# Kernel tuning notes

Hardware: AMD Instinct MI355X
Metric: run time of the kernel (lower is better)

## Reference

```python
import jax, jax.numpy as jnp
import numpy as np

MODE = 'max'  # matches init kwarg `mode`
EPS = 1e-6

def before_after(x):
    n, d = x.shape
    zero = jnp.zeros((1, d), dtype=x.dtype)
    if MODE == 'max':
        # exclusive prefix max (x_before[0] = 0, matching torch.zeros_like base)
        pre = jax.lax.cummax(x, axis=0)
        before = jnp.concatenate([zero, pre[:-1]], axis=0)
        suf = jax.lax.cummax(x[::-1], axis=0)[::-1]
        after = jnp.concatenate([suf[1:], zero], axis=0)
    else:  # mean
        cs = jnp.cumsum(x, axis=0)
        cnt_b = jnp.arange(1, n, dtype=x.dtype)[:, None]
        before = jnp.concatenate([zero, cs[:-1] / cnt_b], axis=0)
        total = cs[-1]
        cnt_a = jnp.arange(n - 1, 0, -1, dtype=x.dtype)[:, None]
        after = jnp.concatenate([(total[None, :] - cs[:-1]) / cnt_a, zero], axis=0)
    return before, after

def setup_inputs() -> dict:
    key = jax.random.key(0)
    ks = jax.random.split(key, 6)
    n, dim, dff = 8192, 1024, 4096
    s1 = 1.0 / np.sqrt(3 * dim)
    s2 = 1.0 / np.sqrt(dff)
    return {
        'x': jax.random.normal(ks[0], (n, dim), jnp.float32),
        'W1': jax.random.normal(ks[1], (dff, 3 * dim), jnp.float32) * s1,
        'b1': jax.random.normal(ks[2], (dff,), jnp.float32) * s1,
        'ln_w': jnp.ones((dff,), jnp.float32),
        'ln_b': jnp.zeros((dff,), jnp.float32),
        'W2': jax.random.normal(ks[3], (dim, dff), jnp.float32) * s2,
        'b2': jax.random.normal(ks[4], (dim,), jnp.float32) * s2,
        'gamma': jnp.full((dim,), 1e-6, jnp.float32),
    }

def reference(x, W1, b1, ln_w, ln_b, W2, b2, gamma):
    shortcut = x
    before, after = before_after(x)
    h = jnp.concatenate([x, before, after], axis=1)          # [n, 3*dim]
    h = jax.nn.relu(h @ W1.T + b1)                           # [n, dff]
    mu = jnp.mean(h, axis=-1, keepdims=True)
    var = jnp.mean(jnp.square(h - mu), axis=-1, keepdims=True)
    h = (h - mu) * jax.lax.rsqrt(var + EPS) * ln_w + ln_b
    # dropout is identity in eval mode
    out = h @ W2.T + b2                                      # [n, dim]
    return out * gamma[None, :] + shortcut
```

## Files before the change

kernel.cpp:

```cpp
#include <hip/hip_runtime.h>

typedef __attribute__((ext_vector_type(4))) float f32x4;
typedef __attribute__((ext_vector_type(8))) short s16x8;
typedef __attribute__((ext_vector_type(8))) unsigned short u16x8;

#define AS1(p) ((const __attribute__((address_space(1))) void*)(p))
#define AS3(p) ((__attribute__((address_space(3))) void*)(p))

__device__ __forceinline__ unsigned short f2bf(float f) {
  unsigned u = __builtin_bit_cast(unsigned, f);
  u += 0x7fffu + ((u >> 16) & 1u);
  return (unsigned short)(u >> 16);
}
__device__ __forceinline__ float bf2f(unsigned short s) {
  unsigned u = ((unsigned)s) << 16;
  return __builtin_bit_cast(float, u);
}
__device__ __forceinline__ unsigned f2e4m3(float f) {
  unsigned uf = __builtin_bit_cast(unsigned, f);
  unsigned s = (uf >> 24) & 0x80u;
  unsigned u = uf & 0x7fffffffu;
  if (u < 0x3c800000u) return s;
  if (u > 0x43e00000u) u = 0x43e00000u;
  u += 0x7ffffu + ((u >> 20) & 1u);
  unsigned v = (u >> 20) - 960u;
  if (v > 126u) v = 126u;
  return s | v;
}


__global__ __launch_bounds__(256) void cast_weights(const float* __restrict__ W1,
                                                    unsigned char* __restrict__ W1q,
                                                    long n1,
                                                    const float* __restrict__ W2,
                                                    unsigned char* __restrict__ W2q,
                                                    long n2) {
  if (blockIdx.x < 1536) {
    long i = ((long)blockIdx.x * 256 + threadIdx.x) * 4;
    long stride = (long)1536 * 256 * 4;
    for (; i < n1; i += stride) {
      float4 f = *(const float4*)(W1 + i);
      unsigned v = f2e4m3(f.x * 32.f) | (f2e4m3(f.y * 32.f) << 8) |
                   (f2e4m3(f.z * 32.f) << 16) | (f2e4m3(f.w * 32.f) << 24);
      long n = i / 3072;
      long k = i - n * 3072;
      long phys = n * 3072 + (k & ~(long)127) + ((k & 127) ^ ((n & 15) << 3));
      *(unsigned*)(W1q + phys) = v;
    }
  } else {
    long i = ((long)(blockIdx.x - 1536) * 256 + threadIdx.x) * 4;
    long stride = (long)512 * 256 * 4;
    for (; i < n2; i += stride) {
      float4 f = *(const float4*)(W2 + i);
      unsigned v = f2e4m3(f.x * 32.f) | (f2e4m3(f.y * 32.f) << 8) |
                   (f2e4m3(f.z * 32.f) << 16) | (f2e4m3(f.w * 32.f) << 24);
      long n = i >> 12;
      long k = i & 4095;
      long phys = (n << 12) + (k & ~(long)127) + ((k & 127) ^ ((n & 15) << 3));
      *(unsigned*)(W2q + phys) = v;
    }
  }
}

__global__ __launch_bounds__(256) void w2_fold(const float* __restrict__ W2,
                                               const float* __restrict__ lnw,
                                               const float* __restrict__ lnb,
                                               float* __restrict__ w2l,
                                               float* __restrict__ b2l) {
  const int n = blockIdx.x;
  const float* w = W2 + (long)n * 4096;
  float s = 0.f, b = 0.f;
  for (int k = threadIdx.x; k < 4096; k += 256) {
    float wv = w[k];
    s += wv * lnw[k];
    b += wv * lnb[k];
  }
#pragma unroll
  for (int off = 32; off; off >>= 1) {
    s += __shfl_xor(s, off, 64);
    b += __shfl_xor(b, off, 64);
  }
  __shared__ float ss[4], bb[4];
  const int wv2 = threadIdx.x >> 6;
  if ((threadIdx.x & 63) == 0) { ss[wv2] = s; bb[wv2] = b; }
  __syncthreads();
  if (threadIdx.x == 0) {
    w2l[n] = ss[0] + ss[1] + ss[2] + ss[3];
    b2l[n] = bb[0] + bb[1] + bb[2] + bb[3];
  }
}

__global__ __launch_bounds__(256) void scan_chunkmax(const float* __restrict__ x,
                                                     float* __restrict__ partial) {
  int col = blockIdx.x * 256 + threadIdx.x;
  int chunk = blockIdx.y;
  const float* p = x + (long)chunk * 64 * 1024 + col;
  float m = -INFINITY;
#pragma unroll 4
  for (int i = 0; i < 64; i++) m = fmaxf(m, p[(long)i * 1024]);
  partial[chunk * 1024 + col] = m;
}

__global__ __launch_bounds__(256) void scan_chunkscan(const float* __restrict__ partial,
                                                      float* __restrict__ prefix,
                                                      float* __restrict__ suffix) {
  int col = blockIdx.x * 256 + threadIdx.x;
  float v[128];
#pragma unroll
  for (int c = 0; c < 128; c++) v[c] = partial[c * 1024 + col];
  float run = -INFINITY;
#pragma unroll
  for (int c = 0; c < 128; c++) {
    prefix[c * 1024 + col] = run;
    run = fmaxf(run, v[c]);
  }
  run = -INFINITY;
#pragma unroll
  for (int c = 127; c >= 0; c--) {
    suffix[c * 1024 + col] = run;
    run = fmaxf(run, v[c]);
  }
}

__global__ __launch_bounds__(256) void scan_emit(const float* __restrict__ x,
                                                 const float* __restrict__ prefix,
                                                 const float* __restrict__ suffix,
                                                 unsigned char* __restrict__ h_in) {
  int col = blockIdx.x * 256 + threadIdx.x;
  int chunk = blockIdx.y;
  long r0 = (long)chunk * 64;
  const int cb = col & ~127, cw = col & 127;
  float run = prefix[chunk * 1024 + col];
  for (int i = 0; i < 64; i++) {
    long row = r0 + i;
    int xo = (int)(row & 15) << 3;
    int c0 = cb | (cw ^ xo);
    float v = x[row * 1024 + col];
    unsigned char* hr = h_in + row * 3072;
    hr[c0] = (unsigned char)f2e4m3(v);
    hr[1024 + c0] = (unsigned char)(row == 0 ? 0u : f2e4m3(run));
    run = fmaxf(run, v);
  }
  float run2 = suffix[chunk * 1024 + col];
  for (int i = 63; i >= 0; i--) {
    long row = r0 + i;
    int xo = (int)(row & 15) << 3;
    int c0 = cb | (cw ^ xo);
    float v = x[row * 1024 + col];
    h_in[row * 3072 + 2048 + c0] = (unsigned char)(row == 8191 ? 0u : f2e4m3(run2));
    run2 = fmaxf(run2, v);
  }
}

__global__ __launch_bounds__(256) void ln_stats_reduce(const float* __restrict__ pp,
                                                       float* __restrict__ rowstats) {
  int row = blockIdx.x * 256 + threadIdx.x;
  int tm = row >> 8, rl = row & 255;
  float s = 0.f, q = 0.f;
#pragma unroll
  for (int tn = 0; tn < 16; ++tn) {
    const float* p = pp + (((long)(tm * 16 + tn) * 256 + rl) * 2);
    s += p[0];
    q += p[1];
  }
  float mu = s * (1.f / 4096.f);
  float var = q * (1.f / 4096.f) - mu * mu;
  rowstats[row * 2] = mu;
  rowstats[row * 2 + 1] = rsqrtf(var + 1e-6f);
}

__global__ __launch_bounds__(512, 2) void gemm256_relu(
    const unsigned char* __restrict__ A, const unsigned char* __restrict__ B,
    unsigned char* __restrict__ C, const float* __restrict__ bias,
    const float* __restrict__ lnw, float* __restrict__ pp,
    int M, int N, int K) {
  extern __shared__ char smem[];
  const int NT = K >> 7;

  const int nwg = gridDim.x;
  const int cpx = nwg >> 3;
  const int bid = blockIdx.x;
  const int swz = (bid & 7) * cpx + (bid >> 3);
  const int tiles_m = M >> 8;
  const int tm = swz % tiles_m;
  const int tn = swz / tiles_m;
  const long brow = (long)tm * 256;
  const long bcol = (long)tn * 256;

  const int t = threadIdx.x;
  const int lane = t & 63, wv = t >> 6;
  const int wr = wv >> 2, wc = wv & 3;
  const int fr = lane & 15, fk = lane >> 4;

  const int srow = t >> 3;
  const int scol = (t & 7) * 16;
  const unsigned char* Asrc = A + (brow + srow) * (long)K + scol;
  const unsigned char* Bsrc = B + (bcol + srow) * (long)K + scol;
  const long hstep = (long)128 * K, lstep = (long)64 * K;

#define STAGE_A(j, reg, h, L)                                                   \
  __builtin_amdgcn_global_load_lds(AS1(Asrc + (h)*hstep + (L)*lstep + (j)*128), \
      AS3(smem + (reg)*32768 + (h)*16384 + (L)*8192 + t * 16), 16, 0, 0)
#define STAGE_B(j, h, L)                                                        \
  __builtin_amdgcn_global_load_lds(AS1(Bsrc + (h)*hstep + (L)*lstep + (j)*128), \
      AS3(smem + 98304 + ((j)&1) * 32768 + (h)*16384 + (L)*8192 + t * 16), 16, 0, 0)

  const int xr = fr << 3;
  const char* ArdRow = smem + (wr * 128 + fr) * 128;
  const char* BrdRow = smem + 98304 + (wc * 64 + fr) * 128;
#define RD_A(ar_, m, kk) \
  (*(const long*)(ArdRow + (ar_)*32768 + (m)*2048 + (((kk)*32 + fk * 8) ^ xr)))
#define RD_B(pb_, n, kk) \
  (*(const long*)(BrdRow + (pb_)*32768 + (n)*2048 + (((kk)*32 + fk * 8) ^ xr)))

#define MFMA_QUAD(mi, a_)                                                      \
  _Pragma("unroll")                                                            \
  for (int n = 0; n < 4; ++n) {                                                \
    _Pragma("unroll")                                                          \
    for (int kk = 0; kk < 4; ++kk)                                             \
      acc[(mi)][n] = __builtin_amdgcn_mfma_f32_16x16x32_fp8_fp8(               \
          a_[kk], bfr[n][kk], acc[(mi)][n], 0, 0, 0);                          \
  }

  f32x4 acc[8][4];
#pragma unroll
  for (int m = 0; m < 8; m++)
#pragma unroll
    for (int n = 0; n < 4; n++) acc[m][n] = (f32x4)0.f;

  STAGE_A(0, 0, 0, 0); STAGE_A(0, 0, 0, 1); STAGE_A(0, 0, 1, 0); STAGE_A(0, 0, 1, 1);
  STAGE_B(0, 0, 0); STAGE_B(0, 0, 1); STAGE_B(0, 1, 0); STAGE_B(0, 1, 1);
  STAGE_A(1, 1, 0, 0); STAGE_A(1, 1, 0, 1); STAGE_A(1, 1, 1, 0); STAGE_A(1, 1, 1, 1);
  STAGE_B(1, 0, 0); STAGE_B(1, 0, 1); STAGE_B(1, 1, 0); STAGE_B(1, 1, 1);
  asm volatile("s_waitcnt vmcnt(8)" ::: "memory");
  __builtin_amdgcn_s_barrier();

  long bfr[4][4];
  long ap[2][2][4];
  ap[0][0][0] = RD_A(0, 0, 0); ap[0][0][1] = RD_A(0, 0, 1);
  ap[0][0][2] = RD_A(0, 0, 2); ap[0][0][3] = RD_A(0, 0, 3);
  ap[0][1][0] = RD_A(0, 1, 0); ap[0][1][1] = RD_A(0, 1, 1);
  ap[0][1][2] = RD_A(0, 1, 2); ap[0][1][3] = RD_A(0, 1, 3);

  int ar = 0;
  for (int g = 0; g < NT; ++g) {
    const int pb = g & 1;
    int sr = ar + 2; if (sr >= 3) sr -= 3;
    int nar = ar + 1; if (nar >= 3) nar = 0;
    const bool st = (g + 2 < NT);
#pragma unroll
    for (int p = 0; p < 4; ++p) {
      const int cs = p & 1, ns = cs ^ 1;
      if (p == 0) {
#pragma unroll
        for (int n = 0; n < 4; ++n)
#pragma unroll
          for (int kk = 0; kk < 4; ++kk) bfr[n][kk] = RD_B(pb, n, kk);
      }
      asm volatile("s_waitcnt lgkmcnt(0)" ::: "memory");
      __builtin_amdgcn_sched_barrier(0);
      __builtin_amdgcn_s_setprio(1);
      MFMA_QUAD(2 * p, ap[cs][0])
      MFMA_QUAD(2 * p + 1, ap[cs][1])
      __builtin_amdgcn_s_setprio(0);
      if (p < 3) {
#pragma unroll
        for (int kk = 0; kk < 4; ++kk) {
          ap[ns][0][kk] = RD_A(ar, 2 * p + 2, kk);
          ap[ns][1][kk] = RD_A(ar, 2 * p + 3, kk);
        }
      } else if (g + 1 < NT) {
#pragma unroll
        for (int kk = 0; kk < 4; ++kk) {
          ap[ns][0][kk] = RD_A(nar, 0, kk);
          ap[ns][1][kk] = RD_A(nar, 1, kk);
        }
      }
      if (st) {
        if (p == 0) { STAGE_A(g + 2, sr, 0, 0); STAGE_A(g + 2, sr, 0, 1); }
        if (p == 1) { STAGE_A(g + 2, sr, 1, 0); STAGE_A(g + 2, sr, 1, 1); }
        if (p == 2) { STAGE_B(g + 2, 0, 0); STAGE_B(g + 2, 0, 1); }
        if (p == 3) { STAGE_B(g + 2, 1, 0); STAGE_B(g + 2, 1, 1); }
      }
      if (p == 2 && g + 1 < NT) {
        if (st) asm volatile("s_waitcnt vmcnt(6)" ::: "memory");
        else    asm volatile("s_waitcnt vmcnt(0)" ::: "memory");
      }
      asm volatile("s_barrier" ::: "memory");
    }
    ar = nar;
  }

  float bi[4], lw[4];
#pragma unroll
  for (int n = 0; n < 4; ++n) {
    const long col = bcol + wc * 64 + n * 16 + fr;
    bi[n] = bias[col];
    lw[n] = lnw[col];
  }
  float* sred = (float*)smem;
  float* qred = sred + 1024;
  const long orow = brow + wr * 128 + fk * 4;
  const int ocol = (int)bcol + wc * 64 + fr;
#pragma unroll
  for (int m = 0; m < 8; ++m) {
#pragma unroll
    for (int r = 0; r < 4; ++r) {
      const long row = orow + m * 16 + r;
      const int xo = ((fk * 4 + r) & 15) << 3;
      float s = 0.f, q = 0.f;
#pragma unroll
      for (int n = 0; n < 4; ++n) {
        float v = acc[m][n][r] * 0.03125f + bi[n];
        v = v > 0.f ? v : 0.f;
        s += v;
        q += v * v;
        const int col = ocol + n * 16;
        const int phys = (col & ~127) | ((col & 127) ^ xo);
        C[row * (long)N + phys] = (unsigned char)f2e4m3(v * lw[n]);
      }
#pragma unroll
      for (int off = 1; off < 16; off <<= 1) {
        s += __shfl_xor(s, off, 64);
        q += __shfl_xor(q, off, 64);
      }
      if (fr == 0) {
        int rl = wr * 128 + m * 16 + fk * 4 + r;
        sred[rl * 4 + wc] = s;
        qred[rl * 4 + wc] = q;
      }
    }
  }
  __syncthreads();
  if (t < 256) {
    float s = sred[t * 4] + sred[t * 4 + 1] + sred[t * 4 + 2] + sred[t * 4 + 3];
    float q = qred[t * 4] + qred[t * 4 + 1] + qred[t * 4 + 2] + qred[t * 4 + 3];
    float* pb = pp + (((long)(tm * 16 + tn) * 256 + t) * 2);
    pb[0] = s;
    pb[1] = q;
  }
#undef STAGE_A
#undef STAGE_B
#undef RD_A
#undef RD_B
#undef MFMA_QUAD
}

__global__ __launch_bounds__(512, 2) void gemm256_g2(
    const unsigned char* __restrict__ A, const unsigned char* __restrict__ B,
    float* __restrict__ Cf, const float* __restrict__ bias,
    const float* __restrict__ gamma, const float* __restrict__ resid,
    const float* __restrict__ w2l, const float* __restrict__ b2l,
    const float* __restrict__ rowstats,
    int M, int N, int K) {
  extern __shared__ char smem[];
  const int NT = K >> 7;

  const int nwg = gridDim.x;
  const int cpx = nwg >> 3;
  const int bid = blockIdx.x;
  const int swz = (bid & 7) * cpx + (bid >> 3);
  const int tiles_m = M >> 8;
  const int tm = swz % tiles_m;
  const int tn = swz / tiles_m;
  const long brow = (long)tm * 256;
  const long bcol = (long)tn * 128;

  const int t = threadIdx.x;
  const int lane = t & 63, wv = t >> 6;
  const int wr = wv >> 1, wc = wv & 1;
  const int fr = lane & 15, fk = lane >> 4;

  const int srow = t >> 3;
  const int scol = (t & 7) * 16;
  const unsigned char* Asrc = A + (brow + srow) * (long)K + scol;
  const unsigned char* Bsrc = B + (bcol + srow) * (long)K + scol;
  const long hstep = (long)128 * K, lstep = (long)64 * K;

#define STAGE_A2(j, reg, h, L)                                                  \
  __builtin_amdgcn_global_load_lds(AS1(Asrc + (h)*hstep + (L)*lstep + (j)*128), \
      AS3(smem + (reg)*32768 + (h)*16384 + (L)*8192 + t * 16), 16, 0, 0)
#define STAGE_B2(j, L)                                                          \
  __builtin_amdgcn_global_load_lds(AS1(Bsrc + (L)*lstep + (j)*128),             \
      AS3(smem + 98304 + ((j)&1) * 16384 + (L)*8192 + t * 16), 16, 0, 0)

  const int xr = fr << 3;
  const char* ArdRow = smem + (wr * 64 + fr) * 128;
  const char* BrdRow = smem + 98304 + (wc * 64 + fr) * 128;
#define RD_A2(ar_, m, kk) \
  (*(const long*)(ArdRow + (ar_)*32768 + (m)*2048 + (((kk)*32 + fk * 8) ^ xr)))
#define RD_B2(pb_, n, kk) \
  (*(const long*)(BrdRow + (pb_)*16384 + (n)*2048 + (((kk)*32 + fk * 8) ^ xr)))

  f32x4 acc[4][4];
#pragma unroll
  for (int m = 0; m < 4; m++)
#pragma unroll
    for (int n = 0; n < 4; n++) acc[m][n] = (f32x4)0.f;

  STAGE_A2(0, 0, 0, 0); STAGE_A2(0, 0, 0, 1); STAGE_A2(0, 0, 1, 0); STAGE_A2(0, 0, 1, 1);
  STAGE_B2(0, 0); STAGE_B2(0, 1);
  STAGE_A2(1, 1, 0, 0); STAGE_A2(1, 1, 0, 1); STAGE_A2(1, 1, 1, 0); STAGE_A2(1, 1, 1, 1);
  STAGE_B2(1, 0); STAGE_B2(1, 1);
  asm volatile("s_waitcnt vmcnt(6)" ::: "memory");
  __builtin_amdgcn_s_barrier();

  long bfr[4][4];
  long ap[2][4];
  ap[0][0] = RD_A2(0, 0, 0); ap[0][1] = RD_A2(0, 0, 1);
  ap[0][2] = RD_A2(0, 0, 2); ap[0][3] = RD_A2(0, 0, 3);

  int ar = 0;
  for (int g = 0; g < NT; ++g) {
    const int pb = g & 1;
    int sr = ar + 2; if (sr >= 3) sr -= 3;
    int nar = ar + 1; if (nar >= 3) nar = 0;
    const bool st = (g + 2 < NT);
#pragma unroll
    for (int p = 0; p < 4; ++p) {
      const int cs = p & 1, ns = cs ^ 1;
      if (p == 0) {
#pragma unroll
        for (int n = 0; n < 4; ++n)
#pragma unroll
          for (int kk = 0; kk < 4; ++kk) bfr[n][kk] = RD_B2(pb, n, kk);
      }
      asm volatile("s_waitcnt lgkmcnt(0)" ::: "memory");
      __builtin_amdgcn_sched_barrier(0);
      __builtin_amdgcn_s_setprio(1);
#pragma unroll
      for (int n = 0; n < 4; ++n)
#pragma unroll
        for (int kk = 0; kk < 4; ++kk)
          acc[p][n] = __builtin_amdgcn_mfma_f32_16x16x32_fp8_fp8(
              ap[cs][kk], bfr[n][kk], acc[p][n], 0, 0, 0);
      __builtin_amdgcn_s_setprio(0);
      if (p < 3) {
#pragma unroll
        for (int kk = 0; kk < 4; ++kk) ap[ns][kk] = RD_A2(ar, p + 1, kk);
      } else if (g + 1 < NT) {
#pragma unroll
        for (int kk = 0; kk < 4; ++kk) ap[ns][kk] = RD_A2(nar, 0, kk);
      }
      if (st) {
        if (p == 0) { STAGE_A2(g + 2, sr, 0, 0); STAGE_A2(g + 2, sr, 0, 1); }
        if (p == 1) { STAGE_A2(g + 2, sr, 1, 0); STAGE_A2(g + 2, sr, 1, 1); }
        if (p == 2) { STAGE_B2(g + 2, 0); STAGE_B2(g + 2, 1); }
      }
      if (p == 2 && g + 1 < NT) {
        if (st) asm volatile("s_waitcnt vmcnt(6)" ::: "memory");
        else    asm volatile("s_waitcnt vmcnt(0)" ::: "memory");
      }
      asm volatile("s_barrier" ::: "memory");
    }
    ar = nar;
  }

  float bi[4], ga[4], wl[4], bl[4];
#pragma unroll
  for (int n = 0; n < 4; ++n) {
    const long col = bcol + wc * 64 + n * 16 + fr;
    bi[n] = bias[col];
    ga[n] = gamma[col];
    wl[n] = w2l[col];
    bl[n] = b2l[col];
  }
  const long orow = brow + wr * 64 + fk * 4;
  const long ocol = bcol + wc * 64 + fr;
#pragma unroll
  for (int m = 0; m < 4; ++m)
#pragma unroll
    for (int r = 0; r < 4; ++r) {
      const long row = orow + m * 16 + r;
      const float mu = rowstats[row * 2];
      const float rs = rowstats[row * 2 + 1];
#pragma unroll
      for (int n = 0; n < 4; ++n) {
        const long col = ocol + n * 16;
        float v = rs * (acc[m][n][r] * 0.03125f) - rs * mu * wl[n] + bl[n] + bi[n];
        Cf[row * (long)N + col] = v * ga[n] + resid[row * (long)N + col];
      }
    }
#undef STAGE_A2
#undef STAGE_B2
#undef RD_A2
#undef RD_B2
}

extern "C" void kernel_launch(void* const* d_in, const int* in_sizes, int n_in,
                              void* d_out, int out_size, void* d_ws, size_t ws_size,
                              hipStream_t stream) {
  const float* x     = (const float*)d_in[0];
  const float* W1    = (const float*)d_in[1];
  const float* b1    = (const float*)d_in[2];
  const float* ln_w  = (const float*)d_in[3];
  const float* ln_b  = (const float*)d_in[4];
  const float* W2    = (const float*)d_in[5];
  const float* b2    = (const float*)d_in[6];
  const float* gamma = (const float*)d_in[7];
  float* out = (float*)d_out;

  const int Nr = 8192, DIM = 1024, DFF = 4096, K1 = 3072;

  unsigned char* W1q   = (unsigned char*)d_ws;
  unsigned char* W2q   = W1q + (long)DFF * K1;
  unsigned char* h_in  = W2q + (long)DIM * DFF;
  unsigned char* h_act = h_in + (long)Nr * K1;
  float* partial  = (float*)(h_act + (long)Nr * DFF);
  float* prefix   = partial + 128 * 1024;
  float* suffix   = prefix + 128 * 1024;
  float* pp       = suffix + 128 * 1024;
  float* rowstats = pp + 32 * 16 * 256 * 2;
  float* w2l      = rowstats + (long)Nr * 2;
  float* b2l      = w2l + DIM;

  hipFuncSetAttribute((const void*)gemm256_relu,
                      hipFuncAttributeMaxDynamicSharedMemorySize, 163840);
  hipFuncSetAttribute((const void*)gemm256_g2,
                      hipFuncAttributeMaxDynamicSharedMemorySize, 131072);

  cast_weights<<<2048, 256, 0, stream>>>(W1, W1q, (long)DFF * K1,
                                         W2, W2q, (long)DIM * DFF);

  scan_chunkmax<<<dim3(4, 128), 256, 0, stream>>>(x, partial);
  scan_chunkscan<<<4, 256, 0, stream>>>(partial, prefix, suffix);
  scan_emit<<<dim3(4, 128), 256, 0, stream>>>(x, prefix, suffix, h_in);

  w2_fold<<<DIM, 256, 0, stream>>>(W2, ln_w, ln_b, w2l, b2l);

  gemm256_relu<<<512, 512, 163840, stream>>>(h_in, W1q, h_act, b1, ln_w, pp,
                                             Nr, DFF, K1);

  ln_stats_reduce<<<32, 256, 0, stream>>>(pp, rowstats);

  gemm256_g2<<<256, 512, 131072, stream>>>(h_act, W2q, out, b2, gamma, x,
                                           w2l, b2l, rowstats, Nr, DIM, DFF);
}
```

Baseline: 297.2 us.

## Merge prep kernels and fold scan and LN-stats reduction into consumers

Combines weight casting, chunk-max, and W2 LayerNorm folding into one prep launch. The chunk-level prefix/suffix scan is dropped: each scan_emit thread now reads all 128 chunk partials and computes its own exclusive prefix and suffix max. The separate LN-stats reduction kernel is removed, and the second GEMM reduces per-row partial sums into shared memory in its epilogue. This cuts the launch count from 8 to 4 and removes small serial kernels, at the cost of redundant partial reads in scan_emit and a block barrier in the GEMM epilogue.

```diff
diff --git a/kernel.cpp b/kernel.cpp
--- a/kernel.cpp
+++ b/kernel.cpp
@@ -1,8 +1,6 @@
 #include <hip/hip_runtime.h>
 
 typedef __attribute__((ext_vector_type(4))) float f32x4;
-typedef __attribute__((ext_vector_type(8))) short s16x8;
-typedef __attribute__((ext_vector_type(8))) unsigned short u16x8;
 
 #define AS1(p) ((const __attribute__((address_space(1))) void*)(p))
 #define AS3(p) ((__attribute__((address_space(3))) void*)(p))
@@ -11,10 +9,6 @@
   unsigned u = __builtin_bit_cast(unsigned, f);
   u += 0x7fffu + ((u >> 16) & 1u);
   return (unsigned short)(u >> 16);
-}
-__device__ __forceinline__ float bf2f(unsigned short s) {
-  unsigned u = ((unsigned)s) << 16;
-  return __builtin_bit_cast(float, u);
 }
 __device__ __forceinline__ unsigned f2e4m3(float f) {
   unsigned uf = __builtin_bit_cast(unsigned, f);
@@ -29,15 +23,22 @@
 }
 
 
-__global__ __launch_bounds__(256) void cast_weights(const float* __restrict__ W1,
-                                                    unsigned char* __restrict__ W1q,
-                                                    long n1,
-                                                    const float* __restrict__ W2,
-                                                    unsigned char* __restrict__ W2q,
-                                                    long n2) {
-  if (blockIdx.x < 1536) {
-    long i = ((long)blockIdx.x * 256 + threadIdx.x) * 4;
-    long stride = (long)1536 * 256 * 4;
+__global__ __launch_bounds__(256) void prep(const float* __restrict__ W1,
+                                            unsigned char* __restrict__ W1q,
+                                            const float* __restrict__ W2,
+                                            unsigned char* __restrict__ W2q,
+                                            const float* __restrict__ x,
+                                            float* __restrict__ partial,
+                                            const float* __restrict__ lnw,
+                                            const float* __restrict__ lnb,
+                                            float* __restrict__ w2l,
+                                            float* __restrict__ b2l) {
+  __shared__ float ss[4], bb[4];
+  const int bid = blockIdx.x;
+  if (bid < 1536) {
+    long i = ((long)bid * 256 + threadIdx.x) * 4;
+    const long n1 = (long)4096 * 3072;
+    const long stride = (long)1536 * 256 * 4;
     for (; i < n1; i += stride) {
       float4 f = *(const float4*)(W1 + i);
       unsigned v = f2e4m3(f.x * 32.f) | (f2e4m3(f.y * 32.f) << 8) |
@@ -47,9 +48,10 @@
       long phys = n * 3072 + (k & ~(long)127) + ((k & 127) ^ ((n & 15) << 3));
       *(unsigned*)(W1q + phys) = v;
     }
-  } else {
-    long i = ((long)(blockIdx.x - 1536) * 256 + threadIdx.x) * 4;
-    long stride = (long)512 * 256 * 4;
+  } else if (bid < 2048) {
+    long i = ((long)(bid - 1536) * 256 + threadIdx.x) * 4;
+    const long n2 = (long)1024 * 4096;
+    const long stride = (long)512 * 256 * 4;
     for (; i < n2; i += stride) {
       float4 f = *(const float4*)(W2 + i);
       unsigned v = f2e4m3(f.x * 32.f) | (f2e4m3(f.y * 32.f) << 8) |
@@ -59,78 +61,54 @@
       long phys = (n << 12) + (k & ~(long)127) + ((k & 127) ^ ((n & 15) << 3));
       *(unsigned*)(W2q + phys) = v;
     }
-  }
-}
-
-__global__ __launch_bounds__(256) void w2_fold(const float* __restrict__ W2,
-                                               const float* __restrict__ lnw,
-                                               const float* __restrict__ lnb,
-                                               float* __restrict__ w2l,
-                                               float* __restrict__ b2l) {
-  const int n = blockIdx.x;
-  const float* w = W2 + (long)n * 4096;
-  float s = 0.f, b = 0.f;
-  for (int k = threadIdx.x; k < 4096; k += 256) {
-    float wv = w[k];
-    s += wv * lnw[k];
-    b += wv * lnb[k];
-  }
-#pragma unroll
-  for (int off = 32; off; off >>= 1) {
-    s += __shfl_xor(s, off, 64);
-    b += __shfl_xor(b, off, 64);
-  }
-  __shared__ float ss[4], bb[4];
-  const int wv2 = threadIdx.x >> 6;
-  if ((threadIdx.x & 63) == 0) { ss[wv2] = s; bb[wv2] = b; }
-  __syncthreads();
-  if (threadIdx.x == 0) {
-    w2l[n] = ss[0] + ss[1] + ss[2] + ss[3];
-    b2l[n] = bb[0] + bb[1] + bb[2] + bb[3];
-  }
-}
-
-__global__ __launch_bounds__(256) void scan_chunkmax(const float* __restrict__ x,
-                                                     float* __restrict__ partial) {
-  int col = blockIdx.x * 256 + threadIdx.x;
-  int chunk = blockIdx.y;
-  const float* p = x + (long)chunk * 64 * 1024 + col;
-  float m = -INFINITY;
+  } else if (bid < 2560) {
+    const int b = bid - 2048;
+    const int col = (b & 3) * 256 + threadIdx.x;
+    const int chunk = b >> 2;
+    const float* p = x + (long)chunk * 64 * 1024 + col;
+    float m = -INFINITY;
 #pragma unroll 4
-  for (int i = 0; i < 64; i++) m = fmaxf(m, p[(long)i * 1024]);
-  partial[chunk * 1024 + col] = m;
-}
-
-__global__ __launch_bounds__(256) void scan_chunkscan(const float* __restrict__ partial,
-                                                      float* __restrict__ prefix,
-                                                      float* __restrict__ suffix) {
-  int col = blockIdx.x * 256 + threadIdx.x;
-  float v[128];
-#pragma unroll
-  for (int c = 0; c < 128; c++) v[c] = partial[c * 1024 + col];
-  float run = -INFINITY;
-#pragma unroll
-  for (int c = 0; c < 128; c++) {
-    prefix[c * 1024 + col] = run;
-    run = fmaxf(run, v[c]);
-  }
-  run = -INFINITY;
-#pragma unroll
-  for (int c = 127; c >= 0; c--) {
-    suffix[c * 1024 + col] = run;
-    run = fmaxf(run, v[c]);
+    for (int i = 0; i < 64; i++) m = fmaxf(m, p[(long)i * 1024]);
+    partial[chunk * 1024 + col] = m;
+  } else {
+    const int n = bid - 2560;
+    const float* w = W2 + (long)n * 4096;
+    float s = 0.f, b = 0.f;
+    for (int k = threadIdx.x; k < 4096; k += 256) {
+      float wv = w[k];
+      s += wv * lnw[k];
+      b += wv * lnb[k];
+    }
+#pragma unroll
+    for (int off = 32; off; off >>= 1) {
+      s += __shfl_xor(s, off, 64);
+      b += __shfl_xor(b, off, 64);
+    }
+    const int wv2 = threadIdx.x >> 6;
+    if ((threadIdx.x & 63) == 0) { ss[wv2] = s; bb[wv2] = b; }
+    __syncthreads();
+    if (threadIdx.x == 0) {
+      w2l[n] = ss[0] + ss[1] + ss[2] + ss[3];
+      b2l[n] = bb[0] + bb[1] + bb[2] + bb[3];
+    }
   }
 }
 
 __global__ __launch_bounds__(256) void scan_emit(const float* __restrict__ x,
-                                                 const float* __restrict__ prefix,
-                                                 const float* __restrict__ suffix,
+                                                 const float* __restrict__ partial,
                                                  unsigned char* __restrict__ h_in) {
-  int col = blockIdx.x * 256 + threadIdx.x;
-  int chunk = blockIdx.y;
+  const int col = blockIdx.x * 256 + threadIdx.x;
+  const int chunk = blockIdx.y;
+  float pre = -INFINITY, suf = -INFINITY;
+#pragma unroll
+  for (int c = 0; c < 128; ++c) {
+    float pv = partial[c * 1024 + col];
+    if (c < chunk) pre = fmaxf(pre, pv);
+    if (c > chunk) suf = fmaxf(suf, pv);
+  }
   long r0 = (long)chunk * 64;
   const int cb = col & ~127, cw = col & 127;
-  float run = prefix[chunk * 1024 + col];
+  float run = pre;
   for (int i = 0; i < 64; i++) {
     long row = r0 + i;
     int xo = (int)(row & 15) << 3;
@@ -141,7 +119,7 @@
     hr[1024 + c0] = (unsigned char)(row == 0 ? 0u : f2e4m3(run));
     run = fmaxf(run, v);
   }
-  float run2 = suffix[chunk * 1024 + col];
+  float run2 = suf;
   for (int i = 63; i >= 0; i--) {
     long row = r0 + i;
     int xo = (int)(row & 15) << 3;
@@ -150,23 +128,6 @@
     h_in[row * 3072 + 2048 + c0] = (unsigned char)(row == 8191 ? 0u : f2e4m3(run2));
     run2 = fmaxf(run2, v);
   }
-}
-
-__global__ __launch_bounds__(256) void ln_stats_reduce(const float* __restrict__ pp,
-                                                       float* __restrict__ rowstats) {
-  int row = blockIdx.x * 256 + threadIdx.x;
-  int tm = row >> 8, rl = row & 255;
-  float s = 0.f, q = 0.f;
-#pragma unroll
-  for (int tn = 0; tn < 16; ++tn) {
-    const float* p = pp + (((long)(tm * 16 + tn) * 256 + rl) * 2);
-    s += p[0];
-    q += p[1];
-  }
-  float mu = s * (1.f / 4096.f);
-  float var = q * (1.f / 4096.f) - mu * mu;
-  rowstats[row * 2] = mu;
-  rowstats[row * 2 + 1] = rsqrtf(var + 1e-6f);
 }
 
 __global__ __launch_bounds__(512, 2) void gemm256_relu(
@@ -351,7 +312,7 @@
     float* __restrict__ Cf, const float* __restrict__ bias,
     const float* __restrict__ gamma, const float* __restrict__ resid,
     const float* __restrict__ w2l, const float* __restrict__ b2l,
-    const float* __restrict__ rowstats,
+    const float* __restrict__ pp,
     int M, int N, int K) {
   extern __shared__ char smem[];
   const int NT = K >> 7;
@@ -456,6 +417,22 @@
     ar = nar;
   }
 
+  float* stats = (float*)smem;
+  if (t < 256) {
+    float s = 0.f, q = 0.f;
+#pragma unroll
+    for (int tb = 0; tb < 16; ++tb) {
+      const float* p = pp + (((long)(tm * 16 + tb) * 256 + t) * 2);
+      s += p[0];
+      q += p[1];
+    }
+    float mu = s * (1.f / 4096.f);
+    float var = q * (1.f / 4096.f) - mu * mu;
+    stats[t * 2] = mu;
+    stats[t * 2 + 1] = rsqrtf(var + 1e-6f);
+  }
+  __syncthreads();
+
   float bi[4], ga[4], wl[4], bl[4];
 #pragma unroll
   for (int n = 0; n < 4; ++n) {
@@ -467,13 +444,15 @@
   }
   const long orow = brow + wr * 64 + fk * 4;
   const long ocol = bcol + wc * 64 + fr;
+  const int rl0 = wr * 64 + fk * 4;
 #pragma unroll
   for (int m = 0; m < 4; ++m)
 #pragma unroll
     for (int r = 0; r < 4; ++r) {
       const long row = orow + m * 16 + r;
-      const float mu = rowstats[row * 2];
-      const float rs = rowstats[row * 2 + 1];
+      const int rl = rl0 + m * 16 + r;
+      const float mu = stats[rl * 2];
+      const float rs = stats[rl * 2 + 1];
 #pragma unroll
       for (int n = 0; n < 4; ++n) {
         const long col = ocol + n * 16;
@@ -506,33 +485,23 @@
   unsigned char* W2q   = W1q + (long)DFF * K1;
   unsigned char* h_in  = W2q + (long)DIM * DFF;
   unsigned char* h_act = h_in + (long)Nr * K1;
-  float* partial  = (float*)(h_act + (long)Nr * DFF);
-  float* prefix   = partial + 128 * 1024;
-  float* suffix   = prefix + 128 * 1024;
-  float* pp       = suffix + 128 * 1024;
-  float* rowstats = pp + 32 * 16 * 256 * 2;
-  float* w2l      = rowstats + (long)Nr * 2;
-  float* b2l      = w2l + DIM;
+  float* partial = (float*)(h_act + (long)Nr * DFF);
+  float* pp      = partial + 128 * 1024;
+  float* w2l     = pp + 32 * 16 * 256 * 2;
+  float* b2l     = w2l + DIM;
 
   hipFuncSetAttribute((const void*)gemm256_relu,
                       hipFuncAttributeMaxDynamicSharedMemorySize, 163840);
   hipFuncSetAttribute((const void*)gemm256_g2,
                       hipFuncAttributeMaxDynamicSharedMemorySize, 131072);
 
-  cast_weights<<<2048, 256, 0, stream>>>(W1, W1q, (long)DFF * K1,
-                                         W2, W2q, (long)DIM * DFF);
-
-  scan_chunkmax<<<dim3(4, 128), 256, 0, stream>>>(x, partial);
-  scan_chunkscan<<<4, 256, 0, stream>>>(partial, prefix, suffix);
-  scan_emit<<<dim3(4, 128), 256, 0, stream>>>(x, prefix, suffix, h_in);
-
-  w2_fold<<<DIM, 256, 0, stream>>>(W2, ln_w, ln_b, w2l, b2l);
+  prep<<<3584, 256, 0, stream>>>(W1, W1q, W2, W2q, x, partial, ln_w, ln_b, w2l, b2l);
+
+  scan_emit<<<dim3(4, 128), 256, 0, stream>>>(x, partial, h_in);
 
   gemm256_relu<<<512, 512, 163840, stream>>>(h_in, W1q, h_act, b1, ln_w, pp,
                                              Nr, DFF, K1);
 
-  ln_stats_reduce<<<32, 256, 0, stream>>>(pp, rowstats);
-
   gemm256_g2<<<256, 512, 131072, stream>>>(h_act, W2q, out, b2, gamma, x,
-                                           w2l, b2l, rowstats, Nr, DIM, DFF);
-}
+                                           w2l, b2l, pp, Nr, DIM, DFF);
+}
```

Measured after the change: 282.9 us, median of 2. -4.8%, faster.
